# Optimization experiments

Hardware: AMD Instinct MI355X
Metric: run time of the kernel (lower is better)

Reference implementation:

```python
import jax, jax.numpy as jnp
import numpy as np

N = 50000
E = 800000
IN_DIM, HID, OUT = 128, 64, 64
SLOPE = 0.2  # PyG GATConv default negative_slope


def gat_conv(x, W, a_src, a_dst, b, src, dst):
    """Single-head PyG GATConv, add_self_loops=False."""
    h = x @ W                                  # [N, F]
    alpha_s = h @ a_src                        # [N]
    alpha_d = h @ a_dst                        # [N]
    e = jax.nn.leaky_relu(alpha_s[src] + alpha_d[dst], SLOPE)   # [E]
    # segment softmax over incoming edges of each destination node
    m = jax.ops.segment_max(e, dst, num_segments=N)             # [N]
    w = jnp.exp(e - m[dst])                                     # [E]
    z = jax.ops.segment_sum(w, dst, num_segments=N)             # [N]
    alpha = w / z[dst]                                          # [E]
    out = jax.ops.segment_sum(h[src] * alpha[:, None], dst, num_segments=N)
    return out + b


def setup_inputs() -> dict:
    key = jax.random.key(0)
    ks = jax.random.split(key, 12)
    x = jax.random.normal(ks[0], (N, IN_DIM), dtype=jnp.float32)
    edge_index = jax.random.randint(ks[1], (2, E), 0, N, dtype=jnp.int64)
    s1 = 1.0 / np.sqrt(IN_DIM)
    s2 = 1.0 / np.sqrt(HID)
    return {
        "x": x,
        "edge_index": edge_index,
        "W1": jax.random.normal(ks[2], (IN_DIM, HID), dtype=jnp.float32) * s1,
        "att_src1": jax.random.normal(ks[3], (HID,), dtype=jnp.float32) * s2,
        "att_dst1": jax.random.normal(ks[4], (HID,), dtype=jnp.float32) * s2,
        "b1": jnp.zeros((HID,), dtype=jnp.float32),
        "W2": jax.random.normal(ks[5], (HID, OUT), dtype=jnp.float32) * s2,
        "att_src2": jax.random.normal(ks[6], (OUT,), dtype=jnp.float32) / np.sqrt(OUT),
        "att_dst2": jax.random.normal(ks[7], (OUT,), dtype=jnp.float32) / np.sqrt(OUT),
        "b2": jnp.zeros((OUT,), dtype=jnp.float32),
    }


def reference(x, edge_index, W1, att_src1, att_dst1, b1, W2, att_src2, att_dst2, b2):
    src, dst = edge_index[0], edge_index[1]
    h = gat_conv(x, W1, att_src1, att_dst1, b1, src, dst)
    h = jax.nn.relu(h)
    # dropout is identity in eval mode
    h = gat_conv(h, W2, att_src2, att_dst2, b2, src, dst)
    # F.normalize(p=2, dim=-1): divide by max(norm, eps)
    norm = jnp.linalg.norm(h, axis=-1, keepdims=True)
    return h / jnp.maximum(norm, 1e-12)
```

## Files before the change

kernel.cpp:

```cpp
#include <hip/hip_runtime.h>
#include <hip/hip_fp16.h>
#include <math.h>

#define NNODES 50000
#define NEDGES 800000
#define NBUCK 256
#define EPB 8192
#define NBLK1 ((NEDGES + EPB - 1) / EPB)
#define SCANL (NBUCK * NBLK1)
#define SCANB ((SCANL + 1023) / 1024)
#define FCAP 8192
#define NGEMM1 ((NNODES + 63) / 64)


__global__ __launch_bounds__(256) void k_bcount(const int* __restrict__ dst,
                                                int* __restrict__ bcnt) {
    __shared__ int h[NBUCK];
    int t = threadIdx.x, b = blockIdx.x;
    h[t] = 0;
    __syncthreads();
    const int4* d4 = (const int4*)dst;
    int beg = b * (EPB / 4), end = min(beg + EPB / 4, NEDGES / 4);
    for (int e = beg + t; e < end; e += 256) {
        int4 v = d4[e];
        atomicAdd(&h[v.x >> 8], 1);
        atomicAdd(&h[v.y >> 8], 1);
        atomicAdd(&h[v.z >> 8], 1);
        atomicAdd(&h[v.w >> 8], 1);
    }
    __syncthreads();
    bcnt[t * NBLK1 + b] = h[t];
}

__global__ void k_scan_block(const int* __restrict__ in, int* __restrict__ out,
                             int* __restrict__ partial, int n) {
    __shared__ int tmp[1024];
    int t = threadIdx.x;
    int i = blockIdx.x * 1024 + t;
    int v = (i < n) ? in[i] : 0;
    tmp[t] = v;
    __syncthreads();
    for (int off = 1; off < 1024; off <<= 1) {
        int u = (t >= off) ? tmp[t - off] : 0;
        __syncthreads();
        tmp[t] += u;
        __syncthreads();
    }
    if (i < n) out[i] = tmp[t] - v;
    if (t == 1023) partial[blockIdx.x] = tmp[t];
}

__device__ __forceinline__ void scan_partials(const int* __restrict__ partial, int* sp) {
    int t = threadIdx.x;
    if (t < 64) {
        int v = (t < SCANB) ? partial[t] : 0;
        int incl = v;
        #pragma unroll
        for (int off = 1; off < 64; off <<= 1) {
            int u = __shfl_up(incl, off, 64);
            if (t >= off) incl += u;
        }
        if (t < SCANB) sp[t] = incl - v;
    }
    __syncthreads();
}


__device__ __forceinline__ void fma4(float4& a, float s, const float4& w) {
    a.x = fmaf(s, w.x, a.x);
    a.y = fmaf(s, w.y, a.y);
    a.z = fmaf(s, w.z, a.z);
    a.w = fmaf(s, w.w, a.w);
}

template<int K, int XH>
__device__ __forceinline__ void gemm_body(
    float* __restrict__ Xs, float* __restrict__ Ws, int bid,
    const void* __restrict__ Xv, const float* __restrict__ W,
    const float* __restrict__ a_src, const float* __restrict__ a_dst,
    __half* __restrict__ H, float* __restrict__ AS, float* __restrict__ AD, int N)
{
    constexpr int KF = K / 4;
    constexpr int KFS = (K == 128) ? 5 : 4;
    int t = threadIdx.x;
    int n0 = bid * 64;

    const float4* W4 = (const float4*)W;
    #pragma unroll
    for (int f = t; f < K * 16; f += 256)
        ((float4*)Ws)[f] = W4[f];
    #pragma unroll
    for (int f = t; f < 64 * KF; f += 256) {
        int r = f >> KFS, k4 = f & (KF - 1);
        float4 v = {0.f, 0.f, 0.f, 0.f};
        if (n0 + r < N) {
            if (XH) {
                union { uint2 u; __half2 h2[2]; } c;
                c.u = ((const uint2*)Xv)[(size_t)(n0 + r) * KF + k4];
                float2 lo = __half22float2(c.h2[0]);
                float2 hi = __half22float2(c.h2[1]);
                v = make_float4(lo.x, lo.y, hi.x, hi.y);
            } else {
                v = ((const float4*)Xv)[(size_t)(n0 + r) * KF + k4];
            }
        }
        ((float4*)&Xs[r * K])[k4 ^ ((r >> 2) & 3)] = v;
    }
    __syncthreads();

    int tr = t >> 4, tc = t & 15;
    int xi = tr & 3;
    const float4* xr0 = (const float4*)&Xs[(tr * 4 + 0) * K];
    const float4* xr1 = (const float4*)&Xs[(tr * 4 + 1) * K];
    const float4* xr2 = (const float4*)&Xs[(tr * 4 + 2) * K];
    const float4* xr3 = (const float4*)&Xs[(tr * 4 + 3) * K];
    float4 acc0 = {}, acc1 = {}, acc2 = {}, acc3 = {};

    #pragma unroll 2
    for (int k4 = 0; k4 < KF; ++k4) {
        int sl = k4 ^ xi;
        float4 x0 = xr0[sl], x1 = xr1[sl], x2 = xr2[sl], x3 = xr3[sl];
        float4 w0 = *(const float4*)&Ws[(k4 * 4 + 0) * 64 + tc * 4];
        float4 w1 = *(const float4*)&Ws[(k4 * 4 + 1) * 64 + tc * 4];
        float4 w2 = *(const float4*)&Ws[(k4 * 4 + 2) * 64 + tc * 4];
        float4 w3 = *(const float4*)&Ws[(k4 * 4 + 3) * 64 + tc * 4];
        fma4(acc0, x0.x, w0); fma4(acc0, x0.y, w1); fma4(acc0, x0.z, w2); fma4(acc0, x0.w, w3);
        fma4(acc1, x1.x, w0); fma4(acc1, x1.y, w1); fma4(acc1, x1.z, w2); fma4(acc1, x1.w, w3);
        fma4(acc2, x2.x, w0); fma4(acc2, x2.y, w1); fma4(acc2, x2.z, w2); fma4(acc2, x2.w, w3);
        fma4(acc3, x3.x, w0); fma4(acc3, x3.y, w1); fma4(acc3, x3.z, w2); fma4(acc3, x3.w, w3);
    }

    float4 asv = *(const float4*)&a_src[tc * 4];
    float4 adv = *(const float4*)&a_dst[tc * 4];
    float4 accs[4] = {acc0, acc1, acc2, acc3};
    #pragma unroll
    for (int i = 0; i < 4; ++i) {
        int row = n0 + tr * 4 + i;
        if (row < N) {
            float4 a = accs[i];
            float s1 = a.x * asv.x + a.y * asv.y + a.z * asv.z + a.w * asv.w;
            float s2 = a.x * adv.x + a.y * adv.y + a.z * adv.z + a.w * adv.w;
            #pragma unroll
            for (int o = 1; o < 16; o <<= 1) {
                s1 += __shfl_xor(s1, o, 64);
                s2 += __shfl_xor(s2, o, 64);
            }
            union { __half2 h2[2]; uint2 u; } pk;
            pk.h2[0] = __floats2half2_rn(a.x, a.y);
            pk.h2[1] = __floats2half2_rn(a.z, a.w);
            *(uint2*)&H[(size_t)row * 64 + tc * 4] = pk.u;
            if (tc == 0) { AS[row] = s1; AD[row] = s2; }
        }
    }
}

template<int K, int XH, int MINW>
__global__ __launch_bounds__(256, MINW) void k_gemm_att(
    const void* __restrict__ Xv, const float* __restrict__ W,
    const float* __restrict__ a_src, const float* __restrict__ a_dst,
    __half* __restrict__ H, float* __restrict__ AS, float* __restrict__ AD, int N)
{
    __shared__ float Xs[64 * K];
    __shared__ float Ws[K * 64];
    gemm_body<K, XH>(Xs, Ws, blockIdx.x, Xv, W, a_src, a_dst, H, AS, AD, N);
}


__global__ __launch_bounds__(256, 2) void k_gemm1_bscatter(
    const float* __restrict__ X, const float* __restrict__ W1,
    const float* __restrict__ as1, const float* __restrict__ ad1,
    __half* __restrict__ H, float* __restrict__ AS, float* __restrict__ AD,
    const int* __restrict__ src, const int* __restrict__ dst,
    const int* __restrict__ boffs, const int* __restrict__ partial,
    int* __restrict__ ep)
{
    __shared__ float Xs[64 * 128];
    __shared__ float Ws[128 * 64];
    if (blockIdx.x < NGEMM1) {
        gemm_body<128, 0>(Xs, Ws, blockIdx.x, X, W1, as1, ad1, H, AS, AD, NNODES);
        return;
    }
    int* cur = (int*)Xs;
    int* sp  = (int*)Ws;
    int t = threadIdx.x, b = blockIdx.x - NGEMM1;
    scan_partials(partial, sp);
    int idx = t * NBLK1 + b;
    cur[t] = boffs[idx] + sp[idx >> 10];
    __syncthreads();
    int beg = b * EPB, end = min(beg + EPB, NEDGES);
    for (int e = beg + t; e < end; e += 256) {
        int d = dst[e];
        int pos = atomicAdd(&cur[d >> 8], 1);
        ep[pos] = (src[e] << 8) | (d & 255);
    }
}

__global__ __launch_bounds__(512) void k_fine(const int* __restrict__ ep,
                                              const int* __restrict__ boffs,
                                              const int* __restrict__ partial,
                                              int* __restrict__ offs,
                                              int* __restrict__ esrc) {
    __shared__ int h[NBUCK];
    __shared__ int cur[NBUCK];
    __shared__ int sp[SCANB];
    __shared__ int stg[FCAP];
    __shared__ int srt[FCAP];
    int t = threadIdx.x, buck = blockIdx.x;
    scan_partials(partial, sp);
    int bi = buck * NBLK1;
    int base = boffs[bi] + sp[bi >> 10];
    int endp;
    if (buck == NBUCK - 1) endp = NEDGES;
    else {
        int ei2 = (buck + 1) * NBLK1;
        endp = boffs[ei2] + sp[ei2 >> 10];
    }
    int cnt = endp - base;
    bool fits = (cnt <= FCAP);

    if (t < NBUCK) h[t] = 0;
    __syncthreads();
    if (fits) {
        for (int j = t; j < cnt; j += 512) stg[j] = ep[base + j];
        __syncthreads();
        for (int j = t; j < cnt; j += 512) atomicAdd(&h[stg[j] & 255], 1);
    } else {
        for (int i = base + t; i < endp; i += 512) atomicAdd(&h[ep[i] & 255], 1);
    }
    __syncthreads();
    int v = (t < NBUCK) ? h[t] : 0;
    for (int off = 1; off < 256; off <<= 1) {
        int u = (t >= off && t < NBUCK) ? h[t - off] : 0;
        __syncthreads();
        if (t < NBUCK) h[t] += u;
        __syncthreads();
    }
    if (t < NBUCK) {
        int excl = h[t] - v;
        int node = buck * 256 + t;
        if (node <= NNODES) offs[node] = base + excl;
        cur[t] = excl;
    }
    __syncthreads();
    if (fits) {
        for (int j = t; j < cnt; j += 512) {
            int p = stg[j];
            int pos = atomicAdd(&cur[p & 255], 1);
            srt[pos] = p >> 8;
        }
        __syncthreads();
        for (int j = t; j < cnt; j += 512) esrc[base + j] = srt[j];
    } else {
        for (int i = base + t; i < endp; i += 512) {
            int p = ep[i];
            int pos = atomicAdd(&cur[p & 255], 1);
            esrc[base + pos] = p >> 8;
        }
    }
}

template<int RELU, int NORM, int OUTH>
__global__ __launch_bounds__(256) void k_agg(
    const int* __restrict__ esrc, const int* __restrict__ offs,
    const __half* __restrict__ H, const float* __restrict__ AS,
    const float* __restrict__ AD, const float* __restrict__ bias,
    void* __restrict__ outv, int N)
{
    __shared__ int2 sm[4][64];
    int gid = blockIdx.x * blockDim.x + threadIdx.x;
    int w = gid >> 6;
    int lane = gid & 63;
    int wid = threadIdx.x >> 6;
    int n0 = 2 * w;
    if (n0 >= N) return;
    int half = lane >> 5, fp = lane & 31;
    int nh = n0 + half;
    bool valid = nh < N;
    int beg = valid ? offs[nh] : 0;
    int end = valid ? offs[nh + 1] : 0;
    int deg = end - beg;
    int degO = __shfl_xor(deg, 32, 64);
    int dm = max(deg, degO);
    float2 bp = ((const float2*)bias)[fp];

    if (dm <= 32) {
        float add = valid ? AD[nh] : 0.f;
        int s = 0;
        float logit = -3.0e38f;
        if (fp < deg) {
            s = esrc[beg + fp];
            float l0 = AS[s] + add;
            logit = (l0 > 0.f) ? l0 : 0.2f * l0;
        }
        float m = logit;
        #pragma unroll
        for (int o = 16; o > 0; o >>= 1) m = fmaxf(m, __shfl_xor(m, o, 64));
        float wg = (fp < deg) ? __expf(logit - m) : 0.f;
        float z = wg;
        #pragma unroll
        for (int o = 16; o > 0; o >>= 1) z += __shfl_xor(z, o, 64);
        sm[wid][lane] = make_int2(s, __float_as_int(wg));

        const __half2* H2 = (const __half2*)H;
        float2 a0 = {0.f, 0.f}, a1 = {0.f, 0.f};
        int base = half * 32;
        int k = 0;
        for (; k + 1 < dm; k += 2) {
            int4 v = *(const int4*)&sm[wid][base + k];
            float2 h0 = __half22float2(H2[(size_t)v.x * 32 + fp]);
            float2 h1 = __half22float2(H2[(size_t)v.z * 32 + fp]);
            float w0 = __int_as_float(v.y), w1 = __int_as_float(v.w);
            a0.x = fmaf(w0, h0.x, a0.x); a0.y = fmaf(w0, h0.y, a0.y);
            a1.x = fmaf(w1, h1.x, a1.x); a1.y = fmaf(w1, h1.y, a1.y);
        }
        if (k < dm) {
            int2 v = sm[wid][base + k];
            float2 h0 = __half22float2(H2[(size_t)v.x * 32 + fp]);
            float w0 = __int_as_float(v.y);
            a0.x = fmaf(w0, h0.x, a0.x); a0.y = fmaf(w0, h0.y, a0.y);
        }
        float2 acc = {a0.x + a1.x, a0.y + a1.y};
        float rz = (deg > 0) ? (1.0f / z) : 0.f;
        float2 val2 = make_float2(fmaf(acc.x, rz, bp.x), fmaf(acc.y, rz, bp.y));
        if (RELU) { val2.x = fmaxf(val2.x, 0.f); val2.y = fmaxf(val2.y, 0.f); }
        if (NORM) {
            float ss = val2.x * val2.x + val2.y * val2.y;
            #pragma unroll
            for (int o = 16; o > 0; o >>= 1) ss += __shfl_xor(ss, o, 64);
            float inv = 1.0f / fmaxf(sqrtf(ss), 1e-12f);
            val2.x *= inv; val2.y *= inv;
        }
        if (valid) {
            if (OUTH) ((__half2*)outv)[(size_t)nh * 32 + fp] = __floats2half2_rn(val2.x, val2.y);
            else      ((float2*)outv)[(size_t)nh * 32 + fp] = val2;
        }
        return;
    }

    #pragma unroll 1
    for (int side = 0; side < 2; ++side) {
        int n = n0 + side;
        if (n >= N) break;
        int b2 = offs[n], e2 = offs[n + 1];
        int dg = e2 - b2;
        float add = AD[n];
        if (dg <= 64) {
            int s = 0;
            float logit = -3.0e38f;
            if (lane < dg) {
                s = esrc[b2 + lane];
                float l0 = AS[s] + add;
                logit = (l0 > 0.f) ? l0 : 0.2f * l0;
            }
            float m = logit;
            #pragma unroll
            for (int o = 32; o > 0; o >>= 1) m = fmaxf(m, __shfl_xor(m, o, 64));
            float wg = (lane < dg) ? __expf(logit - m) : 0.f;
            float z = wg;
            #pragma unroll
            for (int o = 32; o > 0; o >>= 1) z += __shfl_xor(z, o, 64);
            sm[wid][lane] = make_int2(s, __float_as_int(wg));
            const __half2* H2 = (const __half2*)H;
            float2 a0 = {0.f, 0.f};
            for (int k = half; k < dg; k += 2) {
                int2 v = sm[wid][k];
                float2 h0 = __half22float2(H2[(size_t)v.x * 32 + fp]);
                float w0 = __int_as_float(v.y);
                a0.x = fmaf(w0, h0.x, a0.x); a0.y = fmaf(w0, h0.y, a0.y);
            }
            a0.x += __shfl_xor(a0.x, 32, 64);
            a0.y += __shfl_xor(a0.y, 32, 64);
            float rz = (dg > 0) ? (1.0f / z) : 0.f;
            float2 val2 = make_float2(fmaf(a0.x, rz, bp.x), fmaf(a0.y, rz, bp.y));
            if (RELU) { val2.x = fmaxf(val2.x, 0.f); val2.y = fmaxf(val2.y, 0.f); }
            if (NORM) {
                float ss = val2.x * val2.x + val2.y * val2.y;
                #pragma unroll
                for (int o = 16; o > 0; o >>= 1) ss += __shfl_xor(ss, o, 64);
                float inv = 1.0f / fmaxf(sqrtf(ss), 1e-12f);
                val2.x *= inv; val2.y *= inv;
            }
            if (half == 0) {
                if (OUTH) ((__half2*)outv)[(size_t)n * 32 + fp] = __floats2half2_rn(val2.x, val2.y);
                else      ((float2*)outv)[(size_t)n * 32 + fp] = val2;
            }
        } else {
            float m = -3.0e38f, z = 0.f, acc = 0.f;
            for (int i = b2; i < e2; ++i) {
                int s = esrc[i];
                float l0 = AS[s] + add;
                l0 = (l0 > 0.f) ? l0 : 0.2f * l0;
                float mn = fmaxf(m, l0);
                float sc = __expf(m - mn);
                float wgt = __expf(l0 - mn);
                z = z * sc + wgt;
                acc = acc * sc + wgt * __half2float(H[(size_t)s * 64 + lane]);
                m = mn;
            }
            float val = acc / z + bias[lane];
            if (RELU) val = fmaxf(val, 0.f);
            if (NORM) {
                float ss = val * val;
                #pragma unroll
                for (int o = 32; o > 0; o >>= 1) ss += __shfl_xor(ss, o, 64);
                val = val / fmaxf(sqrtf(ss), 1e-12f);
            }
            if (OUTH) ((__half*)outv)[(size_t)n * 64 + lane] = __float2half(val);
            else      ((float*)outv)[(size_t)n * 64 + lane] = val;
        }
    }
}


extern "C" void kernel_launch(void* const* d_in, const int* in_sizes, int n_in,
                              void* d_out, int out_size, void* d_ws, size_t ws_size,
                              hipStream_t stream) {
    const float* x   = (const float*)d_in[0];
    const int*   ei  = (const int*)d_in[1];
    const float* W1  = (const float*)d_in[2];
    const float* as1 = (const float*)d_in[3];
    const float* ad1 = (const float*)d_in[4];
    const float* b1  = (const float*)d_in[5];
    const float* W2  = (const float*)d_in[6];
    const float* as2 = (const float*)d_in[7];
    const float* ad2 = (const float*)d_in[8];
    const float* b2  = (const float*)d_in[9];
    const int* src = ei;
    const int* dst = ei + NEDGES;

    char* ws = (char*)d_ws;
    size_t off = 0;
    auto alloc = [&](size_t bytes) -> void* {
        void* p = ws + off;
        off = (off + bytes + 255) & ~(size_t)255;
        return p;
    };
    __half* H    = (__half*)alloc((size_t)NNODES * 64 * 2);
    __half* OUT1 = (__half*)alloc((size_t)NNODES * 64 * 2);
    float* AS    = (float*)alloc((size_t)NNODES * 4);
    float* AD    = (float*)alloc((size_t)NNODES * 4);
    int*   offs  = (int*)alloc((size_t)(NNODES + 1) * 4);
    int*   ep    = (int*)alloc((size_t)NEDGES * 4);
    int*   esrc  = (int*)alloc((size_t)NEDGES * 4);
    int*   bcnt  = (int*)alloc((size_t)SCANL * 4);
    int*   boffs = (int*)alloc((size_t)SCANL * 4);
    int*   part1 = (int*)alloc((size_t)SCANB * 4);

    k_bcount<<<NBLK1, 256, 0, stream>>>(dst, bcnt);
    k_scan_block<<<SCANB, 1024, 0, stream>>>(bcnt, boffs, part1, SCANL);
    k_gemm1_bscatter<<<NGEMM1 + NBLK1, 256, 0, stream>>>(
        x, W1, as1, ad1, H, AS, AD, src, dst, boffs, part1, ep);
    k_fine<<<NBUCK, 512, 0, stream>>>(ep, boffs, part1, offs, esrc);

    int aggBlocks = (NNODES / 2 + 3) / 4;
    k_agg<1, 0, 1><<<aggBlocks, 256, 0, stream>>>(esrc, offs, H, AS, AD, b1, OUT1, NNODES);

    k_gemm_att<64, 1, 3><<<(NNODES + 63) / 64, 256, 0, stream>>>(OUT1, W2, as2, ad2, H, AS, AD, NNODES);
    k_agg<0, 1, 0><<<aggBlocks, 256, 0, stream>>>(esrc, offs, H, AS, AD, b2, d_out, NNODES);
}
```

Measured before the change: 117.0 us.

## Use fp16 MFMA for node-feature GEMMs with pre-swizzled transposed weights

```diff
diff --git a/kernel.cpp b/kernel.cpp
--- a/kernel.cpp
+++ b/kernel.cpp
@@ -12,11 +12,34 @@
 #define FCAP 8192
 #define NGEMM1 ((NNODES + 63) / 64)
 
+typedef _Float16 f16;
+typedef _Float16 f16x4 __attribute__((ext_vector_type(4)));
+typedef _Float16 f16x8 __attribute__((ext_vector_type(8)));
+typedef float    f32x4 __attribute__((ext_vector_type(4)));
+
 
 __global__ __launch_bounds__(256) void k_bcount(const int* __restrict__ dst,
-                                                int* __restrict__ bcnt) {
+                                                int* __restrict__ bcnt,
+                                                const float* __restrict__ W1,
+                                                const float* __restrict__ W2,
+                                                __half* __restrict__ Wt1,
+                                                __half* __restrict__ Wt2) {
     __shared__ int h[NBUCK];
     int t = threadIdx.x, b = blockIdx.x;
+    if (b >= NBLK1) {
+        if (b == NBLK1) {
+            for (int idx = t; idx < 128 * 64; idx += 256) {
+                int k = idx >> 6, col = idx & 63;
+                Wt1[col * 128 + (k ^ ((col & 7) << 3))] = __float2half(W1[idx]);
+            }
+        } else {
+            for (int idx = t; idx < 64 * 64; idx += 256) {
+                int k = idx >> 6, col = idx & 63;
+                Wt2[col * 64 + (k ^ ((col & 7) << 3))] = __float2half(W2[idx]);
+            }
+        }
+        return;
+    }
     h[t] = 0;
     __syncthreads();
     const int4* d4 = (const int4*)dst;
@@ -66,17 +89,10 @@
 }
 
 
-__device__ __forceinline__ void fma4(float4& a, float s, const float4& w) {
-    a.x = fmaf(s, w.x, a.x);
-    a.y = fmaf(s, w.y, a.y);
-    a.z = fmaf(s, w.z, a.z);
-    a.w = fmaf(s, w.w, a.w);
-}
-
 template<int K, int XH>
 __device__ __forceinline__ void gemm_body(
-    float* __restrict__ Xs, float* __restrict__ Ws, int bid,
-    const void* __restrict__ Xv, const float* __restrict__ W,
+    __half* __restrict__ Xs_h, __half* __restrict__ Ws_h, int bid,
+    const void* __restrict__ Xv, const __half* __restrict__ WtSwz,
     const float* __restrict__ a_src, const float* __restrict__ a_dst,
     __half* __restrict__ H, float* __restrict__ AS, float* __restrict__ AD, int N)
 {
@@ -85,99 +101,106 @@
     int t = threadIdx.x;
     int n0 = bid * 64;
 
-    const float4* W4 = (const float4*)W;
-    #pragma unroll
-    for (int f = t; f < K * 16; f += 256)
-        ((float4*)Ws)[f] = W4[f];
+    {
+        const uint2* wsrc = (const uint2*)WtSwz;
+        uint2* wdst = (uint2*)Ws_h;
+        #pragma unroll
+        for (int f = t; f < K * 16; f += 256) wdst[f] = wsrc[f];
+    }
     #pragma unroll
     for (int f = t; f < 64 * KF; f += 256) {
         int r = f >> KFS, k4 = f & (KF - 1);
-        float4 v = {0.f, 0.f, 0.f, 0.f};
+        f16x4 hv = {0, 0, 0, 0};
         if (n0 + r < N) {
             if (XH) {
-                union { uint2 u; __half2 h2[2]; } c;
+                union { uint2 u; f16x4 h4; } c;
                 c.u = ((const uint2*)Xv)[(size_t)(n0 + r) * KF + k4];
-                float2 lo = __half22float2(c.h2[0]);
-                float2 hi = __half22float2(c.h2[1]);
-                v = make_float4(lo.x, lo.y, hi.x, hi.y);
+                hv = c.h4;
             } else {
-                v = ((const float4*)Xv)[(size_t)(n0 + r) * KF + k4];
-            }
-        }
-        ((float4*)&Xs[r * K])[k4 ^ ((r >> 2) & 3)] = v;
-    }
-    __syncthreads();
-
-    int tr = t >> 4, tc = t & 15;
-    int xi = tr & 3;
-    const float4* xr0 = (const float4*)&Xs[(tr * 4 + 0) * K];
-    const float4* xr1 = (const float4*)&Xs[(tr * 4 + 1) * K];
-    const float4* xr2 = (const float4*)&Xs[(tr * 4 + 2) * K];
-    const float4* xr3 = (const float4*)&Xs[(tr * 4 + 3) * K];
-    float4 acc0 = {}, acc1 = {}, acc2 = {}, acc3 = {};
-
-    #pragma unroll 2
-    for (int k4 = 0; k4 < KF; ++k4) {
-        int sl = k4 ^ xi;
-        float4 x0 = xr0[sl], x1 = xr1[sl], x2 = xr2[sl], x3 = xr3[sl];
-        float4 w0 = *(const float4*)&Ws[(k4 * 4 + 0) * 64 + tc * 4];
-        float4 w1 = *(const float4*)&Ws[(k4 * 4 + 1) * 64 + tc * 4];
-        float4 w2 = *(const float4*)&Ws[(k4 * 4 + 2) * 64 + tc * 4];
-        float4 w3 = *(const float4*)&Ws[(k4 * 4 + 3) * 64 + tc * 4];
-        fma4(acc0, x0.x, w0); fma4(acc0, x0.y, w1); fma4(acc0, x0.z, w2); fma4(acc0, x0.w, w3);
-        fma4(acc1, x1.x, w0); fma4(acc1, x1.y, w1); fma4(acc1, x1.z, w2); fma4(acc1, x1.w, w3);
-        fma4(acc2, x2.x, w0); fma4(acc2, x2.y, w1); fma4(acc2, x2.z, w2); fma4(acc2, x2.w, w3);
-        fma4(acc3, x3.x, w0); fma4(acc3, x3.y, w1); fma4(acc3, x3.z, w2); fma4(acc3, x3.w, w3);
-    }
-
-    float4 asv = *(const float4*)&a_src[tc * 4];
-    float4 adv = *(const float4*)&a_dst[tc * 4];
-    float4 accs[4] = {acc0, acc1, acc2, acc3};
+                float4 v = ((const float4*)Xv)[(size_t)(n0 + r) * KF + k4];
+                hv[0] = (f16)v.x; hv[1] = (f16)v.y; hv[2] = (f16)v.z; hv[3] = (f16)v.w;
+            }
+        }
+        int bo = (k4 * 8) ^ ((r & 7) << 4);
+        *(f16x4*)((char*)Xs_h + r * (K * 2) + bo) = hv;
+    }
+    __syncthreads();
+
+    int w = t >> 6, l = t & 63;
+    int lg = l >> 4, l15 = l & 15;
+    int rA = w * 16 + l15;
+    int sw = (l15 & 7) << 4;
+
+    f32x4 acc[4];
     #pragma unroll
-    for (int i = 0; i < 4; ++i) {
-        int row = n0 + tr * 4 + i;
+    for (int ct = 0; ct < 4; ++ct) acc[ct] = (f32x4){0.f, 0.f, 0.f, 0.f};
+
+    const char* pA = (const char*)Xs_h + rA * (K * 2);
+    #pragma unroll
+    for (int ks = 0; ks < K / 32; ++ks) {
+        int ko = ks * 64 + (lg << 4);
+        f16x8 a = *(const f16x8*)(pA + (ko ^ sw));
+        #pragma unroll
+        for (int ct = 0; ct < 4; ++ct) {
+            const char* pB = (const char*)Ws_h + (ct * 16 + l15) * (K * 2) + (ko ^ sw);
+            f16x8 bfr = *(const f16x8*)pB;
+            acc[ct] = __builtin_amdgcn_mfma_f32_16x16x32_f16(a, bfr, acc[ct], 0, 0, 0);
+        }
+    }
+
+    float asv[4], adv[4];
+    #pragma unroll
+    for (int ct = 0; ct < 4; ++ct) {
+        asv[ct] = a_src[ct * 16 + l15];
+        adv[ct] = a_dst[ct * 16 + l15];
+    }
+    #pragma unroll
+    for (int reg = 0; reg < 4; ++reg) {
+        int row = n0 + w * 16 + lg * 4 + reg;
         if (row < N) {
-            float4 a = accs[i];
-            float s1 = a.x * asv.x + a.y * asv.y + a.z * asv.z + a.w * asv.w;
-            float s2 = a.x * adv.x + a.y * adv.y + a.z * adv.z + a.w * adv.w;
+            float s1 = 0.f, s2 = 0.f;
+            #pragma unroll
+            for (int ct = 0; ct < 4; ++ct) {
+                s1 = fmaf(acc[ct][reg], asv[ct], s1);
+                s2 = fmaf(acc[ct][reg], adv[ct], s2);
+            }
             #pragma unroll
             for (int o = 1; o < 16; o <<= 1) {
                 s1 += __shfl_xor(s1, o, 64);
                 s2 += __shfl_xor(s2, o, 64);
             }
-            union { __half2 h2[2]; uint2 u; } pk;
-            pk.h2[0] = __floats2half2_rn(a.x, a.y);
-            pk.h2[1] = __floats2half2_rn(a.z, a.w);
-            *(uint2*)&H[(size_t)row * 64 + tc * 4] = pk.u;
-            if (tc == 0) { AS[row] = s1; AD[row] = s2; }
-        }
-    }
-}
-
-template<int K, int XH, int MINW>
-__global__ __launch_bounds__(256, MINW) void k_gemm_att(
-    const void* __restrict__ Xv, const float* __restrict__ W,
+            #pragma unroll
+            for (int ct = 0; ct < 4; ++ct)
+                H[(size_t)row * 64 + ct * 16 + l15] = __float2half(acc[ct][reg]);
+            if (l15 == 0) { AS[row] = s1; AD[row] = s2; }
+        }
+    }
+}
+
+template<int K, int XH>
+__global__ __launch_bounds__(256, 4) void k_gemm_att(
+    const void* __restrict__ Xv, const __half* __restrict__ WtSwz,
     const float* __restrict__ a_src, const float* __restrict__ a_dst,
     __half* __restrict__ H, float* __restrict__ AS, float* __restrict__ AD, int N)
 {
-    __shared__ float Xs[64 * K];
-    __shared__ float Ws[K * 64];
-    gemm_body<K, XH>(Xs, Ws, blockIdx.x, Xv, W, a_src, a_dst, H, AS, AD, N);
-}
-
-
-__global__ __launch_bounds__(256, 2) void k_gemm1_bscatter(
-    const float* __restrict__ X, const float* __restrict__ W1,
+    __shared__ __align__(16) __half Xs[64 * K];
+    __shared__ __align__(16) __half Ws[64 * K];
+    gemm_body<K, XH>(Xs, Ws, blockIdx.x, Xv, WtSwz, a_src, a_dst, H, AS, AD, N);
+}
+
+
+__global__ __launch_bounds__(256, 4) void k_gemm1_bscatter(
+    const float* __restrict__ X, const __half* __restrict__ Wt1,
     const float* __restrict__ as1, const float* __restrict__ ad1,
     __half* __restrict__ H, float* __restrict__ AS, float* __restrict__ AD,
     const int* __restrict__ src, const int* __restrict__ dst,
     const int* __restrict__ boffs, const int* __restrict__ partial,
     int* __restrict__ ep)
 {
-    __shared__ float Xs[64 * 128];
-    __shared__ float Ws[128 * 64];
+    __shared__ __align__(16) __half Xs[64 * 128];
+    __shared__ __align__(16) __half Ws[64 * 128];
     if (blockIdx.x < NGEMM1) {
-        gemm_body<128, 0>(Xs, Ws, blockIdx.x, X, W1, as1, ad1, H, AS, AD, NNODES);
+        gemm_body<128, 0>(Xs, Ws, blockIdx.x, X, Wt1, as1, ad1, H, AS, AD, NNODES);
         return;
     }
     int* cur = (int*)Xs;
@@ -445,16 +468,18 @@
     int*   bcnt  = (int*)alloc((size_t)SCANL * 4);
     int*   boffs = (int*)alloc((size_t)SCANL * 4);
     int*   part1 = (int*)alloc((size_t)SCANB * 4);
-
-    k_bcount<<<NBLK1, 256, 0, stream>>>(dst, bcnt);
+    __half* Wt1  = (__half*)alloc((size_t)64 * 128 * 2);
+    __half* Wt2  = (__half*)alloc((size_t)64 * 64 * 2);
+
+    k_bcount<<<NBLK1 + 2, 256, 0, stream>>>(dst, bcnt, W1, W2, Wt1, Wt2);
     k_scan_block<<<SCANB, 1024, 0, stream>>>(bcnt, boffs, part1, SCANL);
     k_gemm1_bscatter<<<NGEMM1 + NBLK1, 256, 0, stream>>>(
-        x, W1, as1, ad1, H, AS, AD, src, dst, boffs, part1, ep);
+        x, Wt1, as1, ad1, H, AS, AD, src, dst, boffs, part1, ep);
     k_fine<<<NBUCK, 512, 0, stream>>>(ep, boffs, part1, offs, esrc);
 
     int aggBlocks = (NNODES / 2 + 3) / 4;
     k_agg<1, 0, 1><<<aggBlocks, 256, 0, stream>>>(esrc, offs, H, AS, AD, b1, OUT1, NNODES);
 
-    k_gemm_att<64, 1, 3><<<(NNODES + 63) / 64, 256, 0, stream>>>(OUT1, W2, as2, ad2, H, AS, AD, NNODES);
+    k_gemm_att<64, 1><<<(NNODES + 63) / 64, 256, 0, stream>>>(OUT1, Wt2, as2, ad2, H, AS, AD, NNODES);
     k_agg<0, 1, 0><<<aggBlocks, 256, 0, stream>>>(esrc, offs, H, AS, AD, b2, d_out, NNODES);
 }
```

After: 105.3 us (median of 3 runs). 1.11x faster.
